# Performance work log

Hardware: AMD Instinct MI355X
Metric: run time of the kernel (lower is better)

## Reference

```python
import jax, jax.numpy as jnp
import numpy as np

DIM_IN = 1024
DIM_OUT = 1024
CTX = 2048


def setup_inputs() -> dict:
    key = jax.random.key(0)
    k_x, k_q, k_k, k_v = jax.random.split(key, 4)
    x = jax.random.normal(k_x, (4, CTX, DIM_IN), dtype=jnp.float32)
    # nn.Linear default init ~ U(-1/sqrt(fan_in), 1/sqrt(fan_in)); scale doesn't matter for correctness
    s = 1.0 / np.sqrt(DIM_IN)
    Wq = jax.random.uniform(k_q, (DIM_IN, DIM_OUT), jnp.float32, -s, s)
    Wk = jax.random.uniform(k_k, (DIM_IN, DIM_OUT), jnp.float32, -s, s)
    Wv = jax.random.uniform(k_v, (DIM_IN, DIM_OUT), jnp.float32, -s, s)
    return {"x": x, "Wq": Wq, "Wk": Wk, "Wv": Wv}


def reference(x, Wq, Wk, Wv):
    # x: [B, T, D_in]; W*: [D_in, D_out]
    b, t, _ = x.shape
    q = jnp.einsum('btd,de->bte', x, Wq)
    k = jnp.einsum('btd,de,->bte', x, Wk, jnp.float32(1.0)) if False else jnp.einsum('btd,de->bte', x, Wk)
    v = jnp.einsum('btd,de->bte', x, Wv)
    scores = jnp.einsum('bqe,bke->bqk', q, k)  # [B, T, T]
    causal = jnp.tril(jnp.ones((t, t), dtype=bool))  # True where allowed
    scores = jnp.where(causal, scores, -jnp.inf)
    weights = jax.nn.softmax(scores / jnp.sqrt(jnp.float32(k.shape[-1])), axis=-1)
    # dropout p=0.0 -> identity
    return jnp.einsum('bqk,bke->bqe', weights, v)
```

## Files before the change

### kernel.cpp

```cpp
#include <hip/hip_runtime.h>


using f32x4 = __attribute__((ext_vector_type(4))) float;
using s16x8 = __attribute__((ext_vector_type(8))) short;

#define CTX 2048
#define DIM 1024
#define NB 4

__device__ __forceinline__ short f2bf(float f) {
  union { float f; unsigned u; } v; v.f = f;
  unsigned r = (v.u + 0x7fffu + ((v.u >> 16) & 1u)) >> 16;
  return (short)r;
}

__device__ __forceinline__ void async16(const void* g, void* l) {
  __builtin_amdgcn_global_load_lds(
      (const __attribute__((address_space(1))) void*)g,
      (__attribute__((address_space(3))) void*)l, 16, 0, 0);
}


__global__ __launch_bounds__(256) void cvt_x(const float* __restrict__ in,
                                             short* __restrict__ out, long n8) {
  long i = (long)blockIdx.x * 256 + threadIdx.x;
  if (i >= n8) return;
  const float4* p = (const float4*)in;
  float4 a = p[i * 2], b = p[i * 2 + 1];
  short o[8];
  o[0] = f2bf(a.x); o[1] = f2bf(a.y); o[2] = f2bf(a.z); o[3] = f2bf(a.w);
  o[4] = f2bf(b.x); o[5] = f2bf(b.y); o[6] = f2bf(b.z); o[7] = f2bf(b.w);
  *(int4*)&out[i * 8] = *(int4*)o;
}

__global__ __launch_bounds__(256) void cvt_wT(const float* __restrict__ Wq,
                                              const float* __restrict__ Wk,
                                              const float* __restrict__ Wv,
                                              short* __restrict__ WT) {
  int z = blockIdx.z;
  const float* W = (z == 0) ? Wq : (z == 1) ? Wk : Wv;
  short* o = WT + (long)z * DIM * DIM;
  __shared__ float t[32][33];
  int n0 = blockIdx.x * 32, k0 = blockIdx.y * 32;
  int tx = threadIdx.x, ty = threadIdx.y;
  #pragma unroll
  for (int j = 0; j < 4; ++j)
    t[ty + j * 8][tx] = W[(long)(k0 + ty + j * 8) * DIM + n0 + tx];
  __syncthreads();
  #pragma unroll
  for (int j = 0; j < 4; ++j)
    o[(long)(n0 + ty + j * 8) * DIM + k0 + tx] = f2bf(t[tx][ty + j * 8]);
}

template <int MODE, bool CSKIP, bool KLIM>
__global__ __launch_bounds__(256) void gemm_bt(const short* __restrict__ A,
                                               const short* __restrict__ B,
                                               void* __restrict__ Cout,
                                               int M, int N, int K,
                                               long sA, long sB, long sC, int ldc) {
  const int bx = KLIM ? ((int)gridDim.x - 1 - (int)blockIdx.x) : (int)blockIdx.x;
  const int by = blockIdx.y, bz = blockIdx.z;
  if (CSKIP && by > bx) return;
  const short* Ab = A + bz * sA + (long)bx * 128 * K;
  const short* Bb = B + bz * sB + (long)by * 128 * K;
  __shared__ short As[3][128 * 32];
  __shared__ short Bs[3][128 * 32];
  const int tid = threadIdx.x;
  const int lane = tid & 63, wid = tid >> 6;
  const int wr = wid >> 1, wc = wid & 1;
  const int frow = lane & 15, kgrp = lane >> 4;

  f32x4 acc[4][4];
  const f32x4 zero = {0.f, 0.f, 0.f, 0.f};
  #pragma unroll
  for (int m = 0; m < 4; ++m)
    #pragma unroll
    for (int n = 0; n < 4; ++n) acc[m][n] = zero;

  int kt_end = K >> 5;
  if (KLIM) { int lim = (bx + 1) << 2; if (lim < kt_end) kt_end = lim; }

  const int e0 = wid * 512 + lane * 8;
  const int er = e0 >> 5, ec = e0 & 31;

  #pragma unroll
  for (int t = 0; t < 2; ++t) {
    const int k0 = t << 5;
    #pragma unroll
    for (int p = 0; p < 2; ++p) {
      const int e = e0 + (p << 11);
      const int r = er + (p << 6);
      async16(Ab + (long)r * K + (k0 + ec), &As[t][e]);
      async16(Bb + (long)r * K + (k0 + ec), &Bs[t][e]);
    }
  }

  int cur = 0, stg = 2;
  for (int kt = 0; kt < kt_end; ++kt) {
    if (kt + 1 < kt_end) asm volatile("s_waitcnt vmcnt(4)" ::: "memory");
    else                 asm volatile("s_waitcnt vmcnt(0)" ::: "memory");
    __builtin_amdgcn_s_barrier();
    asm volatile("" ::: "memory");

    if (kt + 2 < kt_end) {
      const int k0n = (kt + 2) << 5;
      #pragma unroll
      for (int p = 0; p < 2; ++p) {
        const int e = e0 + (p << 11);
        const int r = er + (p << 6);
        async16(Ab + (long)r * K + (k0n + ec), &As[stg][e]);
        async16(Bb + (long)r * K + (k0n + ec), &Bs[stg][e]);
      }
    }

    s16x8 af[4], bfr[4];
    #pragma unroll
    for (int m = 0; m < 4; ++m)
      af[m] = *(const s16x8*)&As[cur][((wr << 6) + (m << 4) + frow) * 32 + (kgrp << 3)];
    #pragma unroll
    for (int n = 0; n < 4; ++n)
      bfr[n] = *(const s16x8*)&Bs[cur][((wc << 6) + (n << 4) + frow) * 32 + (kgrp << 3)];
    #pragma unroll
    for (int m = 0; m < 4; ++m)
      #pragma unroll
      for (int n = 0; n < 4; ++n)
        acc[m][n] = __builtin_amdgcn_mfma_f32_16x16x32_bf16(af[m], bfr[n], acc[m][n], 0, 0, 0);

    cur = (cur == 2) ? 0 : cur + 1;
    stg = (stg == 2) ? 0 : stg + 1;
  }

  const int row0 = (bx << 7) + (wr << 6);
  const int col0 = (by << 7) + (wc << 6);
  #pragma unroll
  for (int m = 0; m < 4; ++m) {
    #pragma unroll
    for (int n = 0; n < 4; ++n) {
      #pragma unroll
      for (int r = 0; r < 4; ++r) {
        const int row = row0 + (m << 4) + (kgrp << 2) + r;
        const int col = col0 + (n << 4) + frow;
        const float v = acc[m][n][r];
        if (MODE == 2) {
          ((_Float16*)Cout)[bz * sC + (long)row * ldc + col] = (_Float16)v;
        } else if (MODE == 3) {
          ((float*)Cout)[bz * sC + (long)row * ldc + col] = v;
        } else {
          const long QK = (long)NB * CTX * DIM;
          long off;
          if (col < 2048) {
            off = (long)(col >> 10) * QK + (long)row * DIM + (col & 1023);
          } else {
            off = 2 * QK + (long)(row >> 11) * ((long)DIM * CTX) +
                  (long)(col - 2048) * CTX + (row & (CTX - 1));
          }
          ((short*)Cout)[off] = f2bf(v);
        }
      }
    }
  }
}

__global__ __launch_bounds__(256) void softmax_causal(void* __restrict__ Sbuf) {
  const int r = blockIdx.x, b = blockIdx.y;
  const long base = (long)b * CTX * CTX + (long)r * CTX;
  _Float16* S = (_Float16*)Sbuf + base;
  short* P = (short*)Sbuf + base;
  const int tid = threadIdx.x;
  const int lane = tid & 63, wid = tid >> 6;
  const int c0 = tid * 8;
  const int ncol = ((r >> 7) + 1) << 7;
  const float scale = 0.03125f;

  float v[8];
  if (c0 <= r) {
    _Float16 h[8];
    *(int4*)h = *(const int4*)&S[c0];
    #pragma unroll
    for (int j = 0; j < 8; ++j)
      v[j] = (c0 + j <= r) ? (float)h[j] * scale : -INFINITY;
  } else {
    #pragma unroll
    for (int j = 0; j < 8; ++j) v[j] = -INFINITY;
  }
  float m = -INFINITY;
  #pragma unroll
  for (int j = 0; j < 8; ++j) m = fmaxf(m, v[j]);
  #pragma unroll
  for (int off = 32; off >= 1; off >>= 1) m = fmaxf(m, __shfl_xor(m, off));
  __shared__ float redm[4], reds[4];
  if (lane == 0) redm[wid] = m;
  __syncthreads();
  m = fmaxf(fmaxf(redm[0], redm[1]), fmaxf(redm[2], redm[3]));

  float p[8];
  float s = 0.f;
  #pragma unroll
  for (int j = 0; j < 8; ++j) {
    p[j] = exp2f((v[j] - m) * 1.44269504f);
    s += p[j];
  }
  #pragma unroll
  for (int off = 32; off >= 1; off >>= 1) s += __shfl_xor(s, off);
  if (lane == 0) reds[wid] = s;
  __syncthreads();
  s = reds[0] + reds[1] + reds[2] + reds[3];
  const float inv = 1.0f / s;

  if (c0 < ncol) {
    short o[8];
    #pragma unroll
    for (int j = 0; j < 8; ++j) o[j] = f2bf(p[j] * inv);
    *(int4*)&P[c0] = *(int4*)o;
  }
}

extern "C" void kernel_launch(void* const* d_in, const int* in_sizes, int n_in,
                              void* d_out, int out_size, void* d_ws, size_t ws_size,
                              hipStream_t stream) {
  (void)in_sizes; (void)n_in; (void)out_size; (void)ws_size;
  const float* x  = (const float*)d_in[0];
  const float* Wq = (const float*)d_in[1];
  const float* Wk = (const float*)d_in[2];
  const float* Wv = (const float*)d_in[3];

  const long MB = 1024 * 1024;
  char* ws = (char*)d_ws;
  short* xb = (short*)(ws + 0);
  short* WT = (short*)(ws + 16 * MB);
  short* Qb = (short*)(ws + 24 * MB);
  short* Kb = (short*)(ws + 40 * MB);
  short* Vt = (short*)(ws + 56 * MB);
  void*  S  = (void*)(ws + 72 * MB);

  cvt_x<<<4096, 256, 0, stream>>>(x, xb, (long)NB * CTX * DIM / 8);
  cvt_wT<<<dim3(32, 32, 3), dim3(32, 8), 0, stream>>>(Wq, Wk, Wv, WT);
  gemm_bt<4, false, false><<<dim3(64, 24, 1), 256, 0, stream>>>(
      xb, WT, Qb, NB * CTX, 3 * DIM, DIM, 0, 0, 0, DIM);
  gemm_bt<2, true, false><<<dim3(16, 16, NB), 256, 0, stream>>>(
      Qb, Kb, S, CTX, CTX, DIM, (long)CTX * DIM, (long)CTX * DIM, (long)CTX * CTX, CTX);
  softmax_causal<<<dim3(CTX, NB), 256, 0, stream>>>(S);
  gemm_bt<3, false, true><<<dim3(16, 8, NB), 256, 0, stream>>>(
      (short*)S, Vt, d_out, CTX, DIM, CTX, (long)CTX * CTX, (long)DIM * CTX, (long)CTX * DIM, DIM);
}
```

Baseline: 284.9 us.

## Replace 128x128 GEMM with 256x256 tiled, swizzled-LDS, 8-wave ping-pong GEMM

Replaces the 128x128-tile, 4-wave GEMM with a 256x256-tile, 512-thread kernel that stages BK=64 into double-buffered XOR-swizzled LDS (128KB). It interleaves LDS reads and MFMA quarters between barriers, raising wave priority around the MFMAs. The aim is more data reuse per LDS byte, fewer bank conflicts and better overlap of loads with MFMA. The QKV projection uses a swizzled 1D grid for L2 locality, and the causal tile granularity moves to 256, so softmax writes and PV K-limits widen. The trade-offs are fewer blocks (e.g. 128 for the PV GEMM), single-block occupancy, and more wasted masked work on the causal diagonal.

New measurement: 309.6 us. 8.7% more time.

```diff
diff --git a/kernel.cpp b/kernel.cpp
--- a/kernel.cpp
+++ b/kernel.cpp
@@ -52,107 +52,150 @@
     o[(long)(n0 + ty + j * 8) * DIM + k0 + tx] = f2bf(t[tx][ty + j * 8]);
 }
 
-template <int MODE, bool CSKIP, bool KLIM>
-__global__ __launch_bounds__(256) void gemm_bt(const short* __restrict__ A,
-                                               const short* __restrict__ B,
-                                               void* __restrict__ Cout,
-                                               int M, int N, int K,
-                                               long sA, long sB, long sC, int ldc) {
-  const int bx = KLIM ? ((int)gridDim.x - 1 - (int)blockIdx.x) : (int)blockIdx.x;
-  const int by = blockIdx.y, bz = blockIdx.z;
+#define READ_A(mh)                                                              \
+  do {                                                                          \
+    _Pragma("unroll") for (int mi = 0; mi < 4; ++mi) {                          \
+      _Pragma("unroll") for (int ks = 0; ks < 2; ++ks) {                        \
+        aA[mi][ks] = *(const s16x8*)(smem + abase + laneRd +                    \
+                                     ((mh)*4 + mi) * 2048 + ks * 64);           \
+      }                                                                         \
+    }                                                                           \
+  } while (0)
+
+#define READ_B(nh)                                                              \
+  do {                                                                          \
+    _Pragma("unroll") for (int ni = 0; ni < 2; ++ni) {                          \
+      _Pragma("unroll") for (int ks = 0; ks < 2; ++ks) {                        \
+        bB[ni][ks] = *(const s16x8*)(smem + bbase + laneRd +                    \
+                                     ((nh)*2 + ni) * 2048 + ks * 64);           \
+      }                                                                         \
+    }                                                                           \
+  } while (0)
+
+#define DO_MFMA(mh, nh)                                                         \
+  do {                                                                          \
+    __builtin_amdgcn_s_setprio(1);                                              \
+    _Pragma("unroll") for (int mi = 0; mi < 4; ++mi) {                          \
+      _Pragma("unroll") for (int ni = 0; ni < 2; ++ni) {                        \
+        _Pragma("unroll") for (int ks = 0; ks < 2; ++ks) {                      \
+          acc[(mh)*4 + mi][(nh)*2 + ni] = __builtin_amdgcn_mfma_f32_16x16x32_bf16( \
+              aA[mi][ks], bB[ni][ks], acc[(mh)*4 + mi][(nh)*2 + ni], 0, 0, 0);  \
+        }                                                                       \
+      }                                                                         \
+    }                                                                           \
+    __builtin_amdgcn_s_setprio(0);                                              \
+  } while (0)
+
+template <int MODE, bool CSKIP, bool KLIM, bool SWZGRID>
+__global__ __launch_bounds__(512, 1) void gemm256(const short* __restrict__ A,
+                                                  const short* __restrict__ B,
+                                                  void* __restrict__ Cout,
+                                                  int K, long sA, long sB, long sC,
+                                                  int ldc, int nbx) {
+  int bx, by;
+  if (SWZGRID) {
+    int wg = ((int)blockIdx.x & 7) * ((int)gridDim.x >> 3) + ((int)blockIdx.x >> 3);
+    bx = wg % nbx; by = wg / nbx;
+  } else {
+    bx = blockIdx.x; by = blockIdx.y;
+  }
+  const int bz = blockIdx.z;
   if (CSKIP && by > bx) return;
-  const short* Ab = A + bz * sA + (long)bx * 128 * K;
-  const short* Bb = B + bz * sB + (long)by * 128 * K;
-  __shared__ short As[3][128 * 32];
-  __shared__ short Bs[3][128 * 32];
+
+  const short* Ab = A + bz * sA + (long)bx * 256 * K;
+  const short* Bb = B + bz * sB + (long)by * 256 * K;
+  const long ldb = (long)K * 2;
+
+  __shared__ __align__(16) char smem[131072];
+
   const int tid = threadIdx.x;
   const int lane = tid & 63, wid = tid >> 6;
-  const int wr = wid >> 1, wc = wid & 1;
+  const int wm = wid >> 2, wn = wid & 3;
   const int frow = lane & 15, kgrp = lane >> 4;
-
-  f32x4 acc[4][4];
+  const int xorv = ((frow >> 2) & 1) << 5;
+  const int laneRd = frow * 128 + ((kgrp * 16) ^ xorv);
+  const int sr0 = tid >> 3;
+  const int scb = ((tid & 7) << 4) ^ (((tid >> 5) & 1) << 5);
+
+  int kt_end = K >> 6;
+  if (KLIM) { int lim = (bx + 1) << 2; if (lim < kt_end) kt_end = lim; }
+
+  f32x4 acc[8][4];
   const f32x4 zero = {0.f, 0.f, 0.f, 0.f};
   #pragma unroll
-  for (int m = 0; m < 4; ++m)
-    #pragma unroll
-    for (int n = 0; n < 4; ++n) acc[m][n] = zero;
-
-  int kt_end = K >> 5;
-  if (KLIM) { int lim = (bx + 1) << 2; if (lim < kt_end) kt_end = lim; }
-
-  const int e0 = wid * 512 + lane * 8;
-  const int er = e0 >> 5, ec = e0 & 31;
-
-  #pragma unroll
-  for (int t = 0; t < 2; ++t) {
-    const int k0 = t << 5;
-    #pragma unroll
-    for (int p = 0; p < 2; ++p) {
-      const int e = e0 + (p << 11);
-      const int r = er + (p << 6);
-      async16(Ab + (long)r * K + (k0 + ec), &As[t][e]);
-      async16(Bb + (long)r * K + (k0 + ec), &Bs[t][e]);
-    }
-  }
-
-  int cur = 0, stg = 2;
-  for (int kt = 0; kt < kt_end; ++kt) {
-    if (kt + 1 < kt_end) asm volatile("s_waitcnt vmcnt(4)" ::: "memory");
-    else                 asm volatile("s_waitcnt vmcnt(0)" ::: "memory");
-    __builtin_amdgcn_s_barrier();
-    asm volatile("" ::: "memory");
-
-    if (kt + 2 < kt_end) {
-      const int k0n = (kt + 2) << 5;
+  for (int mi = 0; mi < 8; ++mi)
+    #pragma unroll
+    for (int ni = 0; ni < 4; ++ni) acc[mi][ni] = zero;
+
+  auto STAGE = [&](int bn_, int mat, int tt) {
+    const char* mb = (const char*)(mat ? Bb : Ab) + (long)tt * 128 + scb;
+    #pragma unroll
+    for (int h = 0; h < 2; ++h)
       #pragma unroll
-      for (int p = 0; p < 2; ++p) {
-        const int e = e0 + (p << 11);
-        const int r = er + (p << 6);
-        async16(Ab + (long)r * K + (k0n + ec), &As[stg][e]);
-        async16(Bb + (long)r * K + (k0n + ec), &Bs[stg][e]);
-      }
-    }
-
-    s16x8 af[4], bfr[4];
-    #pragma unroll
-    for (int m = 0; m < 4; ++m)
-      af[m] = *(const s16x8*)&As[cur][((wr << 6) + (m << 4) + frow) * 32 + (kgrp << 3)];
-    #pragma unroll
-    for (int n = 0; n < 4; ++n)
-      bfr[n] = *(const s16x8*)&Bs[cur][((wc << 6) + (n << 4) + frow) * 32 + (kgrp << 3)];
-    #pragma unroll
-    for (int m = 0; m < 4; ++m)
-      #pragma unroll
-      for (int n = 0; n < 4; ++n)
-        acc[m][n] = __builtin_amdgcn_mfma_f32_16x16x32_bf16(af[m], bfr[n], acc[m][n], 0, 0, 0);
-
-    cur = (cur == 2) ? 0 : cur + 1;
-    stg = (stg == 2) ? 0 : stg + 1;
-  }
-
-  const int row0 = (bx << 7) + (wr << 6);
-  const int col0 = (by << 7) + (wc << 6);
-  #pragma unroll
-  for (int m = 0; m < 4; ++m) {
-    #pragma unroll
-    for (int n = 0; n < 4; ++n) {
+      for (int s = 0; s < 2; ++s)
+        async16(mb + (long)(h * 128 + s * 64 + sr0) * ldb,
+                smem + ((bn_ * 2 + mat) * 2 + h) * 16384 + s * 8192 + tid * 16);
+  };
+
+  STAGE(0, 0, 0);
+  STAGE(0, 1, 0);
+  asm volatile("s_waitcnt vmcnt(0)" ::: "memory");
+  __builtin_amdgcn_s_barrier();
+
+  s16x8 aA[4][2], bB[2][2];
+  for (int t = 0; t < kt_end; ++t) {
+    const int buf = t & 1;
+    const int abase = ((buf * 2 + 0) * 2 + wm) * 16384;
+    const int bbase = ((buf * 2 + 1) * 2 + (wn >> 1)) * 16384 + (wn & 1) * 8192;
+    const int bn = buf ^ 1;
+    const bool hn = (t + 1 < kt_end);
+
+    if (hn) STAGE(bn, 0, t + 1);
+    READ_A(0); READ_B(0);
+    __builtin_amdgcn_s_barrier();
+    DO_MFMA(0, 0);
+
+    if (hn) STAGE(bn, 1, t + 1);
+    READ_A(1);
+    __builtin_amdgcn_s_barrier();
+    DO_MFMA(1, 0);
+
+    READ_B(1);
+    __builtin_amdgcn_s_barrier();
+    DO_MFMA(1, 1);
+
+    READ_A(0);
+    __builtin_amdgcn_s_barrier();
+    DO_MFMA(0, 1);
+
+    asm volatile("s_waitcnt vmcnt(0)" ::: "memory");
+    __builtin_amdgcn_s_barrier();
+  }
+
+  const int row0 = bx * 256 + wm * 128;
+  const int col0 = by * 256 + wn * 64;
+  #pragma unroll
+  for (int mi = 0; mi < 8; ++mi) {
+    #pragma unroll
+    for (int ni = 0; ni < 4; ++ni) {
       #pragma unroll
       for (int r = 0; r < 4; ++r) {
-        const int row = row0 + (m << 4) + (kgrp << 2) + r;
-        const int col = col0 + (n << 4) + frow;
-        const float v = acc[m][n][r];
+        const int row = row0 + mi * 16 + kgrp * 4 + r;
+        const int col = col0 + ni * 16 + frow;
+        const float v = acc[mi][ni][r];
         if (MODE == 2) {
           ((_Float16*)Cout)[bz * sC + (long)row * ldc + col] = (_Float16)v;
         } else if (MODE == 3) {
           ((float*)Cout)[bz * sC + (long)row * ldc + col] = v;
         } else {
           const long QK = (long)NB * CTX * DIM;
+          const int colr = col & 1023;
           long off;
           if (col < 2048) {
-            off = (long)(col >> 10) * QK + (long)row * DIM + (col & 1023);
+            off = (long)(col >> 10) * QK + (long)row * DIM + colr;
           } else {
             off = 2 * QK + (long)(row >> 11) * ((long)DIM * CTX) +
-                  (long)(col - 2048) * CTX + (row & (CTX - 1));
+                  (long)colr * CTX + (row & (CTX - 1));
           }
           ((short*)Cout)[off] = f2bf(v);
         }
@@ -169,7 +212,7 @@
   const int tid = threadIdx.x;
   const int lane = tid & 63, wid = tid >> 6;
   const int c0 = tid * 8;
-  const int ncol = ((r >> 7) + 1) << 7;
+  const int ncol = ((r >> 8) + 1) << 8;
   const float scale = 0.03125f;
 
   float v[8];
@@ -235,11 +278,11 @@
 
   cvt_x<<<4096, 256, 0, stream>>>(x, xb, (long)NB * CTX * DIM / 8);
   cvt_wT<<<dim3(32, 32, 3), dim3(32, 8), 0, stream>>>(Wq, Wk, Wv, WT);
-  gemm_bt<4, false, false><<<dim3(64, 24, 1), 256, 0, stream>>>(
-      xb, WT, Qb, NB * CTX, 3 * DIM, DIM, 0, 0, 0, DIM);
-  gemm_bt<2, true, false><<<dim3(16, 16, NB), 256, 0, stream>>>(
-      Qb, Kb, S, CTX, CTX, DIM, (long)CTX * DIM, (long)CTX * DIM, (long)CTX * CTX, CTX);
+  gemm256<4, false, false, true><<<384, 512, 0, stream>>>(
+      xb, WT, Qb, DIM, 0, 0, 0, DIM, 32);
+  gemm256<2, true, false, false><<<dim3(8, 8, NB), 512, 0, stream>>>(
+      Qb, Kb, S, DIM, (long)CTX * DIM, (long)CTX * DIM, (long)CTX * CTX, CTX, 0);
   softmax_causal<<<dim3(CTX, NB), 256, 0, stream>>>(S);
-  gemm_bt<3, false, true><<<dim3(16, 8, NB), 256, 0, stream>>>(
-      (short*)S, Vt, d_out, CTX, DIM, CTX, (long)CTX * CTX, (long)DIM * CTX, (long)CTX * DIM, DIM);
-}
+  gemm256<3, false, true, false><<<dim3(8, 4, NB), 512, 0, stream>>>(
+      (short*)S, Vt, d_out, CTX, (long)CTX * CTX, (long)DIM * CTX, (long)CTX * DIM, DIM, 0);
+}
```
